# Kernel optimization log

Hardware: AMD Instinct MI355X
Metric: run time of the kernel (lower is better)

Reference implementation:

```python
import jax, jax.numpy as jnp
import numpy as np

DF = 16
B, D, H, W = 2, 64, 64, 64


def _shift(a, axis, s):
    """Return a shifted so out[i] = a[i+s] along `axis`, zero-padded."""
    pad = [(0, 0)] * a.ndim
    pad[axis] = (1, 1)
    ap = jnp.pad(a, pad)
    idx = [slice(None)] * a.ndim
    idx[axis] = slice(1 + s, 1 + s + a.shape[axis])
    return ap[tuple(idx)]


def _image_grad(x, sum_axis):
    """Faithful replica of ImageGradient's (buggy) dense kernel.

    Uses only input channel 1; central difference along W; summed over the
    3 taps along `sum_axis` (1=D for pos==1, 2=H for pos==2); result is
    identical across all output channels.
    x: [B, C, D, H, W] -> [B, C, D, H, W]
    """
    s = x[:, 1]  # [B, D, H, W]
    g = 0.5 * (_shift(s, 3, 1) - _shift(s, 3, -1))  # d/dW central diff
    g3 = _shift(g, sum_axis, -1) + g + _shift(g, sum_axis, 1)
    return jnp.broadcast_to(g3[:, None], x.shape)


def _pconv(x, w, b):
    """nn.Conv3d(cin, cout, 1, padding=1): zero-pad spatial dims then 1x1x1 conv."""
    xp = jnp.pad(x, ((0, 0), (0, 0), (1, 1), (1, 1), (1, 1)))
    return jnp.einsum('bcdhw,oc->bodhw', xp, w) + b[None, :, None, None, None]


def setup_inputs() -> dict:
    key = jax.random.key(0)
    ks = jax.random.split(key, 8)
    p = jax.random.normal(ks[0], (B, DF, D, H, W), dtype=jnp.float32)
    q = jax.random.normal(ks[1], (B, DF, D, H, W), dtype=jnp.float32)
    W1 = jax.random.normal(ks[2], (DF, 6 * DF), dtype=jnp.float32) / np.sqrt(6 * DF)
    b1 = jax.random.normal(ks[3], (DF,), dtype=jnp.float32) * 0.01
    W2 = jax.random.normal(ks[4], (DF, DF), dtype=jnp.float32) / np.sqrt(DF)
    b2 = jax.random.normal(ks[5], (DF,), dtype=jnp.float32) * 0.01
    W3 = jax.random.normal(ks[6], (1, DF), dtype=jnp.float32) / np.sqrt(DF)
    b3 = jax.random.normal(ks[7], (1,), dtype=jnp.float32) * 0.01
    return {"p": p, "q": q, "W1": W1, "b1": b1, "W2": W2, "b2": b2, "W3": W3, "b3": b3}


def reference(p, q, W1, b1, W2, b2, W3, b3):
    dpx = _image_grad(p, 1)  # gradx: pos==1, sum over kd (D axis)
    dpy = _image_grad(p, 2)  # grady: pos==2, sum over kh (H axis)
    dqx = _image_grad(q, 1)
    dqy = _image_grad(q, 2)
    h = jnp.concatenate([p, dpx, dpy, q, dqx, dqy], axis=1)  # [B, 6*DF, D, H, W]
    h = jax.nn.relu(_pconv(h, W1, b1))  # [B, DF, D+2, H+2, W+2]
    h = jax.nn.relu(_pconv(h, W2, b2))  # [B, DF, D+4, H+4, W+4]
    h = jax.nn.relu(_pconv(h, W3, b3))  # [B, 1, D+6, H+6, W+6]
    return (h, p, dpx, dpy, q, dqx, dqy)
```

## Files before the change

kernel.cpp:

```cpp
#include <hip/hip_runtime.h>

#define N3   (64*64*64)
#define NO   70
#define NO3  (NO*NO*NO)
#define OH   (2*NO3)
#define SZ   (2*16*N3)

__device__ __forceinline__ float relu(float x){ return x > 0.f ? x : 0.f; }

__global__ __launch_bounds__(256) void ham_fused(
    const float* __restrict__ p, const float* __restrict__ q,
    const float* __restrict__ W1, const float* __restrict__ b1,
    const float* __restrict__ W2, const float* __restrict__ b2,
    const float* __restrict__ W3, const float* __restrict__ b3p,
    float* __restrict__ out)
{
    __shared__ float WpT[16][16];
    __shared__ float WqT[16][16];
    __shared__ float W2l[16][16];
    __shared__ float b1l[16], b2l[16], W3l[16];
    __shared__ float s1x[16], s1y[16], s2x[16], s2y[16];

    int t = threadIdx.x;
    {
        int o = t >> 4, c = t & 15;
        WpT[c][o] = W1[o*96 + c];
        WqT[c][o] = W1[o*96 + 48 + c];
        W2l[o][c] = W2[o*16 + c];
    }
    if (t < 16) {
        b1l[t] = b1[t]; b2l[t] = b2[t]; W3l[t] = W3[t];
        float ax=0.f, ay=0.f, bx=0.f, by=0.f;
        #pragma unroll
        for (int j = 0; j < 16; ++j) {
            ax += W1[t*96 + 16 + j];
            ay += W1[t*96 + 32 + j];
            bx += W1[t*96 + 64 + j];
            by += W1[t*96 + 80 + j];
        }
        s1x[t]=ax; s1y[t]=ay; s2x[t]=bx; s2y[t]=by;
    }
    __syncthreads();

    int idx = blockIdx.x * 256 + t;
    if (idx >= OH) return;

    int b = idx / NO3;
    int r = idx - b*NO3;
    int d = r / (NO*NO); r -= d*(NO*NO);
    int h = r / NO;
    int w = r - h*NO;

    float b3v = b3p[0];
    float outv;

    if ((unsigned)(d-1) >= 68u || (unsigned)(h-1) >= 68u || (unsigned)(w-1) >= 68u) {
        outv = relu(b3v);
    } else {
        float y2[16];
        if ((unsigned)(d-2) >= 66u || (unsigned)(h-2) >= 66u || (unsigned)(w-2) >= 66u) {
            #pragma unroll
            for (int o = 0; o < 16; ++o) y2[o] = relu(b2l[o]);
        } else {
            float y1[16];
            int d0 = d-3, h0 = h-3, w0 = w-3;
            bool interior = (unsigned)d0 < 64u && (unsigned)h0 < 64u && (unsigned)w0 < 64u;
            if (!interior) {
                #pragma unroll
                for (int c = 0; c < 16; ++c) y1[c] = relu(b1l[c]);
            } else {
                const float* ps = p + (b*16 + 1)*N3;
                const float* qs = q + (b*16 + 1)*N3;
                auto ld = [&](const float* s, int dd, int hh, int ww) -> float {
                    if ((unsigned)dd >= 64u || (unsigned)hh >= 64u || (unsigned)ww >= 64u)
                        return 0.f;
                    return s[dd*4096 + hh*64 + ww];
                };
                auto g = [&](const float* s, int dd, int hh, int ww) -> float {
                    return 0.5f*(ld(s, dd, hh, ww+1) - ld(s, dd, hh, ww-1));
                };
                float gcp = g(ps, d0, h0, w0);
                float dpx = g(ps, d0-1, h0, w0) + gcp + g(ps, d0+1, h0, w0);
                float dpy = g(ps, d0, h0-1, w0) + gcp + g(ps, d0, h0+1, w0);
                float gcq = g(qs, d0, h0, w0);
                float dqx = g(qs, d0-1, h0, w0) + gcq + g(qs, d0+1, h0, w0);
                float dqy = g(qs, d0, h0-1, w0) + gcq + g(qs, d0, h0+1, w0);

                #pragma unroll
                for (int o = 0; o < 16; ++o)
                    y1[o] = b1l[o] + s1x[o]*dpx + s1y[o]*dpy + s2x[o]*dqx + s2y[o]*dqy;

                int sbase = d0*4096 + h0*64 + w0;
                int ibase = b*16*N3 + sbase;

                float* outp  = out + OH;
                float* outdx = out + OH + SZ;
                float* outdy = out + OH + 2*SZ;
                float* outq  = out + OH + 3*SZ;
                float* outqx = out + OH + 4*SZ;
                float* outqy = out + OH + 5*SZ;

                #pragma unroll
                for (int c = 0; c < 16; ++c) {
                    float pc = p[ibase + c*N3];
                    float qc = q[ibase + c*N3];
                    outp[ibase + c*N3] = pc;
                    outq[ibase + c*N3] = qc;
                    #pragma unroll
                    for (int o = 0; o < 16; ++o)
                        y1[o] += WpT[c][o]*pc + WqT[c][o]*qc;
                }
                #pragma unroll
                for (int c = 0; c < 16; ++c) {
                    outdx[ibase + c*N3] = dpx;
                    outdy[ibase + c*N3] = dpy;
                    outqx[ibase + c*N3] = dqx;
                    outqy[ibase + c*N3] = dqy;
                }
                #pragma unroll
                for (int o = 0; o < 16; ++o) y1[o] = relu(y1[o]);
            }
            #pragma unroll
            for (int o = 0; o < 16; ++o) {
                float a = b2l[o];
                #pragma unroll
                for (int c = 0; c < 16; ++c) a += W2l[o][c]*y1[c];
                y2[o] = relu(a);
            }
        }
        float a = b3v;
        #pragma unroll
        for (int c = 0; c < 16; ++c) a += W3l[c]*y2[c];
        outv = relu(a);
    }
    out[idx] = outv;
}

extern "C" void kernel_launch(void* const* d_in, const int* in_sizes, int n_in,
                              void* d_out, int out_size, void* d_ws, size_t ws_size,
                              hipStream_t stream) {
    const float* p  = (const float*)d_in[0];
    const float* q  = (const float*)d_in[1];
    const float* W1 = (const float*)d_in[2];
    const float* b1 = (const float*)d_in[3];
    const float* W2 = (const float*)d_in[4];
    const float* b2 = (const float*)d_in[5];
    const float* W3 = (const float*)d_in[6];
    const float* b3 = (const float*)d_in[7];
    float* out = (float*)d_out;

    int total = OH;
    int blocks = (total + 255) / 256;
    ham_fused<<<blocks, 256, 0, stream>>>(p, q, W1, b1, W2, b2, W3, b3, out);
}
```

Measured before the change: 344.5 us.

## Split interior and boundary work, vectorize interior by 4 along W with nontemporal I/O

The kernel now launches two block groups. 512 blocks each handle four consecutive W voxels of the interior using float4 loads and stores, with nontemporal hints on the streaming copies of p and q and on the broadcast gradient outputs. A second group covers the 70^3 output grid but only writes boundary-shell voxels, computed as constants, and skips the interior. This aims to remove per-voxel index divisions and divergence, and to widen memory transactions for the large output writes. The cost is more registers per thread (the y1 array grows to 16x4) and many idle threads in the boundary blocks.

```diff
diff --git a/kernel.cpp b/kernel.cpp
--- a/kernel.cpp
+++ b/kernel.cpp
@@ -2,9 +2,13 @@
 
 #define N3   (64*64*64)
 #define NO   70
+#define NO2  (NO*NO)
 #define NO3  (NO*NO*NO)
 #define OH   (2*NO3)
 #define SZ   (2*16*N3)
+#define NBI  512
+
+typedef float f32x4 __attribute__((ext_vector_type(4)));
 
 __device__ __forceinline__ float relu(float x){ return x > 0.f ? x : 0.f; }
 
@@ -41,99 +45,154 @@
         s1x[t]=ax; s1y[t]=ay; s2x[t]=bx; s2y[t]=by;
     }
     __syncthreads();
-
-    int idx = blockIdx.x * 256 + t;
-    if (idx >= OH) return;
-
-    int b = idx / NO3;
-    int r = idx - b*NO3;
-    int d = r / (NO*NO); r -= d*(NO*NO);
-    int h = r / NO;
-    int w = r - h*NO;
-
     float b3v = b3p[0];
-    float outv;
-
-    if ((unsigned)(d-1) >= 68u || (unsigned)(h-1) >= 68u || (unsigned)(w-1) >= 68u) {
-        outv = relu(b3v);
-    } else {
-        float y2[16];
-        if ((unsigned)(d-2) >= 66u || (unsigned)(h-2) >= 66u || (unsigned)(w-2) >= 66u) {
+
+    if (blockIdx.x >= NBI) {
+        int idx = (blockIdx.x - NBI)*256 + t;
+        if (idx >= OH) return;
+        int b = idx / NO3;
+        int r = idx - b*NO3;
+        int d = r / NO2; r -= d*NO2;
+        int h = r / NO;
+        int w = r - h*NO;
+        int m = min(min(min(d,69-d), min(h,69-h)), min(w,69-w));
+        if (m >= 3) return;
+        float v;
+        if (m == 0) {
+            v = relu(b3v);
+        } else if (m == 1) {
+            float a = b3v;
             #pragma unroll
-            for (int o = 0; o < 16; ++o) y2[o] = relu(b2l[o]);
+            for (int o = 0; o < 16; ++o) a += W3l[o]*relu(b2l[o]);
+            v = relu(a);
         } else {
-            float y1[16];
-            int d0 = d-3, h0 = h-3, w0 = w-3;
-            bool interior = (unsigned)d0 < 64u && (unsigned)h0 < 64u && (unsigned)w0 < 64u;
-            if (!interior) {
-                #pragma unroll
-                for (int c = 0; c < 16; ++c) y1[c] = relu(b1l[c]);
-            } else {
-                const float* ps = p + (b*16 + 1)*N3;
-                const float* qs = q + (b*16 + 1)*N3;
-                auto ld = [&](const float* s, int dd, int hh, int ww) -> float {
-                    if ((unsigned)dd >= 64u || (unsigned)hh >= 64u || (unsigned)ww >= 64u)
-                        return 0.f;
-                    return s[dd*4096 + hh*64 + ww];
-                };
-                auto g = [&](const float* s, int dd, int hh, int ww) -> float {
-                    return 0.5f*(ld(s, dd, hh, ww+1) - ld(s, dd, hh, ww-1));
-                };
-                float gcp = g(ps, d0, h0, w0);
-                float dpx = g(ps, d0-1, h0, w0) + gcp + g(ps, d0+1, h0, w0);
-                float dpy = g(ps, d0, h0-1, w0) + gcp + g(ps, d0, h0+1, w0);
-                float gcq = g(qs, d0, h0, w0);
-                float dqx = g(qs, d0-1, h0, w0) + gcq + g(qs, d0+1, h0, w0);
-                float dqy = g(qs, d0, h0-1, w0) + gcq + g(qs, d0, h0+1, w0);
-
-                #pragma unroll
-                for (int o = 0; o < 16; ++o)
-                    y1[o] = b1l[o] + s1x[o]*dpx + s1y[o]*dpy + s2x[o]*dqx + s2y[o]*dqy;
-
-                int sbase = d0*4096 + h0*64 + w0;
-                int ibase = b*16*N3 + sbase;
-
-                float* outp  = out + OH;
-                float* outdx = out + OH + SZ;
-                float* outdy = out + OH + 2*SZ;
-                float* outq  = out + OH + 3*SZ;
-                float* outqx = out + OH + 4*SZ;
-                float* outqy = out + OH + 5*SZ;
-
-                #pragma unroll
-                for (int c = 0; c < 16; ++c) {
-                    float pc = p[ibase + c*N3];
-                    float qc = q[ibase + c*N3];
-                    outp[ibase + c*N3] = pc;
-                    outq[ibase + c*N3] = qc;
-                    #pragma unroll
-                    for (int o = 0; o < 16; ++o)
-                        y1[o] += WpT[c][o]*pc + WqT[c][o]*qc;
-                }
-                #pragma unroll
-                for (int c = 0; c < 16; ++c) {
-                    outdx[ibase + c*N3] = dpx;
-                    outdy[ibase + c*N3] = dpy;
-                    outqx[ibase + c*N3] = dqx;
-                    outqy[ibase + c*N3] = dqy;
-                }
-                #pragma unroll
-                for (int o = 0; o < 16; ++o) y1[o] = relu(y1[o]);
-            }
+            float a = b3v;
             #pragma unroll
             for (int o = 0; o < 16; ++o) {
-                float a = b2l[o];
+                float s = b2l[o];
                 #pragma unroll
-                for (int c = 0; c < 16; ++c) a += W2l[o][c]*y1[c];
-                y2[o] = relu(a);
+                for (int c = 0; c < 16; ++c) s += W2l[o][c]*relu(b1l[c]);
+                a += W3l[o]*relu(s);
             }
-        }
+            v = relu(a);
+        }
+        out[idx] = v;
+        return;
+    }
+
+    int tid = blockIdx.x*256 + t;
+    int w0 = (tid & 15) << 2;
+    int h0 = (tid >> 4) & 63;
+    int d0 = (tid >> 10) & 63;
+    int b  = tid >> 16;
+
+    const float* ps = p + (b*16 + 1)*N3;
+    const float* qs = q + (b*16 + 1)*N3;
+
+    auto grow = [&](const float* s, int dd, int hh, float g[4]) {
+        if ((unsigned)dd >= 64u || (unsigned)hh >= 64u) {
+            g[0]=g[1]=g[2]=g[3]=0.f; return;
+        }
+        const float* r = s + dd*4096 + hh*64 + w0;
+        f32x4 v = *reinterpret_cast<const f32x4*>(r);
+        float lft = (w0 > 0)  ? r[-1] : 0.f;
+        float rgt = (w0 < 60) ? r[4]  : 0.f;
+        g[0] = 0.5f*(v.y - lft);
+        g[1] = 0.5f*(v.z - v.x);
+        g[2] = 0.5f*(v.w - v.y);
+        g[3] = 0.5f*(rgt - v.z);
+    };
+
+    float gp_c[4], gp_a[4], gp_b[4], gp_e[4], gp_f[4];
+    float gq_c[4], gq_a[4], gq_b[4], gq_e[4], gq_f[4];
+    grow(ps, d0,   h0,   gp_c);
+    grow(ps, d0-1, h0,   gp_a);
+    grow(ps, d0+1, h0,   gp_b);
+    grow(ps, d0,   h0-1, gp_e);
+    grow(ps, d0,   h0+1, gp_f);
+    grow(qs, d0,   h0,   gq_c);
+    grow(qs, d0-1, h0,   gq_a);
+    grow(qs, d0+1, h0,   gq_b);
+    grow(qs, d0,   h0-1, gq_e);
+    grow(qs, d0,   h0+1, gq_f);
+
+    float dpx[4], dpy[4], dqx[4], dqy[4];
+    #pragma unroll
+    for (int j = 0; j < 4; ++j) {
+        dpx[j] = gp_a[j] + gp_c[j] + gp_b[j];
+        dpy[j] = gp_e[j] + gp_c[j] + gp_f[j];
+        dqx[j] = gq_a[j] + gq_c[j] + gq_b[j];
+        dqy[j] = gq_e[j] + gq_c[j] + gq_f[j];
+    }
+
+    float y1[16][4];
+    #pragma unroll
+    for (int o = 0; o < 16; ++o) {
+        #pragma unroll
+        for (int j = 0; j < 4; ++j)
+            y1[o][j] = b1l[o] + s1x[o]*dpx[j] + s1y[o]*dpy[j]
+                              + s2x[o]*dqx[j] + s2y[o]*dqy[j];
+    }
+
+    int sbase = d0*4096 + h0*64 + w0;
+    int ibase = b*16*N3 + sbase;
+
+    float* outp  = out + OH;
+    float* outdx = out + OH + SZ;
+    float* outdy = out + OH + 2*SZ;
+    float* outq  = out + OH + 3*SZ;
+    float* outqx = out + OH + 4*SZ;
+    float* outqy = out + OH + 5*SZ;
+
+    #pragma unroll 4
+    for (int c = 0; c < 16; ++c) {
+        f32x4 pc = __builtin_nontemporal_load(
+                        reinterpret_cast<const f32x4*>(p + ibase + c*N3));
+        f32x4 qc = __builtin_nontemporal_load(
+                        reinterpret_cast<const f32x4*>(q + ibase + c*N3));
+        __builtin_nontemporal_store(pc, reinterpret_cast<f32x4*>(outp + ibase + c*N3));
+        __builtin_nontemporal_store(qc, reinterpret_cast<f32x4*>(outq + ibase + c*N3));
+        #pragma unroll
+        for (int o = 0; o < 16; ++o) {
+            float wp = WpT[c][o], wq = WqT[c][o];
+            y1[o][0] += wp*pc.x + wq*qc.x;
+            y1[o][1] += wp*pc.y + wq*qc.y;
+            y1[o][2] += wp*pc.z + wq*qc.z;
+            y1[o][3] += wp*pc.w + wq*qc.w;
+        }
+    }
+
+    f32x4 vdpx = { dpx[0], dpx[1], dpx[2], dpx[3] };
+    f32x4 vdpy = { dpy[0], dpy[1], dpy[2], dpy[3] };
+    f32x4 vdqx = { dqx[0], dqx[1], dqx[2], dqx[3] };
+    f32x4 vdqy = { dqy[0], dqy[1], dqy[2], dqy[3] };
+    #pragma unroll 4
+    for (int c = 0; c < 16; ++c) {
+        __builtin_nontemporal_store(vdpx, reinterpret_cast<f32x4*>(outdx + ibase + c*N3));
+        __builtin_nontemporal_store(vdpy, reinterpret_cast<f32x4*>(outdy + ibase + c*N3));
+        __builtin_nontemporal_store(vdqx, reinterpret_cast<f32x4*>(outqx + ibase + c*N3));
+        __builtin_nontemporal_store(vdqy, reinterpret_cast<f32x4*>(outqy + ibase + c*N3));
+    }
+
+    #pragma unroll
+    for (int o = 0; o < 16; ++o) {
+        #pragma unroll
+        for (int j = 0; j < 4; ++j) y1[o][j] = relu(y1[o][j]);
+    }
+
+    int hbase = b*NO3 + (d0+3)*NO2 + (h0+3)*NO + (w0+3);
+    #pragma unroll
+    for (int j = 0; j < 4; ++j) {
         float a = b3v;
         #pragma unroll
-        for (int c = 0; c < 16; ++c) a += W3l[c]*y2[c];
-        outv = relu(a);
-    }
-    out[idx] = outv;
+        for (int o = 0; o < 16; ++o) {
+            float s = b2l[o];
+            #pragma unroll
+            for (int c = 0; c < 16; ++c) s += W2l[o][c]*y1[c][j];
+            a += W3l[o]*relu(s);
+        }
+        out[hbase + j] = relu(a);
+    }
 }
 
 extern "C" void kernel_launch(void* const* d_in, const int* in_sizes, int n_in,
@@ -149,7 +208,7 @@
     const float* b3 = (const float*)d_in[7];
     float* out = (float*)d_out;
 
-    int total = OH;
-    int blocks = (total + 255) / 256;
+    int bBoundary = (OH + 255) / 256;
+    int blocks = NBI + bBoundary;
     ham_fused<<<blocks, 256, 0, stream>>>(p, q, W1, b1, W2, b2, W3, b3, out);
 }
```

Result: faster. 310.5 us (-9.9%).
